# Performance work log

Measured on AMD Instinct MI355X. Metric: run time of the kernel, lower is better.

The kernel has to match this reference:

```python
import jax, jax.numpy as jnp
import numpy as np

N = 50000   # nodes
E = 800000  # edges (avg degree 16)
D = 128     # in = hidden = out channels (residual path active)
EPS = 1e-5  # BatchNorm eps


def setup_inputs() -> dict:
    key = jax.random.key(0)
    ks = jax.random.split(key, 24)
    sc = 1.0 / np.sqrt(D)
    inp = {
        "x": jax.random.normal(ks[0], (N, D), jnp.float32),
        "W1": jax.random.normal(ks[1], (D, D), jnp.float32) * sc,
        "b1": jnp.zeros((D,), jnp.float32),
        "g1": 1.0 + 0.1 * jax.random.normal(ks[2], (D,), jnp.float32),
        "be1": 0.1 * jax.random.normal(ks[3], (D,), jnp.float32),
        "m1": 0.1 * jax.random.normal(ks[4], (D,), jnp.float32),
        "v1": 0.5 + jax.random.uniform(ks[5], (D,), jnp.float32),
        "W2": jax.random.normal(ks[6], (D, D), jnp.float32) * sc,
        "b2": jnp.zeros((D,), jnp.float32),
        "g2": 1.0 + 0.1 * jax.random.normal(ks[7], (D,), jnp.float32),
        "be2": 0.1 * jax.random.normal(ks[8], (D,), jnp.float32),
        "m2": 0.1 * jax.random.normal(ks[9], (D,), jnp.float32),
        "v2": 0.5 + jax.random.uniform(ks[10], (D,), jnp.float32),
        "W3": jax.random.normal(ks[11], (D, D), jnp.float32) * sc,
        "b3": jnp.zeros((D,), jnp.float32),
        "src": jax.random.randint(ks[12], (E,), 0, N, jnp.int32),
        "dst": jax.random.randint(ks[13], (E,), 0, N, jnp.int32),
    }
    return inp


def _gcn_conv(x, W, b, src, dst):
    # PyG GCNConv: add self-loops, symmetric D^{-1/2}(A+I)D^{-1/2} normalization.
    h = x @ W                                              # [N, C]
    deg = jax.ops.segment_sum(jnp.ones((E,), x.dtype), dst, num_segments=N) + 1.0
    dinv = jax.lax.rsqrt(deg)                              # [N]
    coef = dinv[src] * dinv[dst]                           # [E]
    agg = jax.ops.segment_sum(h[src] * coef[:, None], dst, num_segments=N)
    agg = agg + h * (dinv * dinv)[:, None]                 # self-loop term
    return agg + b


def _bn(x, g, be, m, v):
    # eval-mode BatchNorm1d with running stats
    return (x - m) * jax.lax.rsqrt(v + EPS) * g + be


def reference(x, W1, b1, g1, be1, m1, v1, W2, b2, g2, be2, m2, v2, W3, b3, src, dst):
    x_res = x
    h = jax.nn.relu(_bn(_gcn_conv(x, W1, b1, src, dst), g1, be1, m1, v1))
    h = jax.nn.relu(_bn(_gcn_conv(h, W2, b2, src, dst), g2, be2, m2, v2))
    h = _gcn_conv(h, W3, b3, src, dst)
    return h + x_res  # in_channels == out_channels -> residual active
```

## Files before the change

### kernel.cpp

```cpp
#include <hip/hip_runtime.h>
#include <hip/hip_bf16.h>


#define GCN_N 50000
#define GCN_E 800000
#define GCN_D 128

__device__ __forceinline__ float bflo(unsigned u) { return __uint_as_float(u << 16); }
__device__ __forceinline__ float bfhi(unsigned u) { return __uint_as_float(u & 0xffff0000u); }
__device__ __forceinline__ unsigned f2bf(float f) {
    unsigned u = __float_as_uint(f);
    return (u + 0x7fffu + ((u >> 16) & 1u)) >> 16;
}

__global__ __launch_bounds__(256) void zero_kernel(int* __restrict__ p, int n) {
    int i = blockIdx.x * blockDim.x + threadIdx.x;
    if (i < n) p[i] = 0;
}

__global__ __launch_bounds__(256) void hist_kernel(const int* __restrict__ dst,
                                                   int* __restrict__ cnt, int nE) {
    int e = blockIdx.x * blockDim.x + threadIdx.x;
    if (e < nE) atomicAdd(&cnt[dst[e]], 1);
}

__global__ __launch_bounds__(256) void block_reduce(const int* __restrict__ cnt,
                                                    int* __restrict__ bsum, int n) {
    int tid = threadIdx.x, lane = tid & 63, wid = tid >> 6;
    int i0 = blockIdx.x * 1024 + tid * 4;
    int s = 0;
    #pragma unroll
    for (int q = 0; q < 4; ++q)
        if (i0 + q < n) s += cnt[i0 + q];
    #pragma unroll
    for (int off = 32; off >= 1; off >>= 1) s += __shfl_xor(s, off);
    __shared__ int ws[4];
    if (lane == 0) ws[wid] = s;
    __syncthreads();
    if (tid == 0) bsum[blockIdx.x] = ws[0] + ws[1] + ws[2] + ws[3];
}

__global__ void scan_bsums(const int* __restrict__ bsum, int* __restrict__ boff,
                           int nb, int* __restrict__ row_last) {
    int lane = threadIdx.x;
    int v = (lane < nb) ? bsum[lane] : 0;
    int sc = v;
    #pragma unroll
    for (int off = 1; off < 64; off <<= 1) {
        int t = __shfl_up(sc, off);
        if (lane >= off) sc += t;
    }
    if (lane < nb) boff[lane] = sc - v;
    if (lane == 63) *row_last = sc;
}

__global__ __launch_bounds__(256) void scan_apply(const int* __restrict__ cnt_in,
                                                  const int* __restrict__ boff,
                                                  int* __restrict__ row_ptr,
                                                  float* __restrict__ dinv,
                                                  int* __restrict__ cnt_zero, int n) {
    __shared__ int wsum[4];
    int tid = threadIdx.x, lane = tid & 63, wid = tid >> 6;
    int i0 = blockIdx.x * 1024 + tid * 4;
    int a0 = 0, a1 = 0, a2 = 0, a3 = 0;
    if (i0 + 0 < n) a0 = cnt_in[i0 + 0];
    if (i0 + 1 < n) a1 = cnt_in[i0 + 1];
    if (i0 + 2 < n) a2 = cnt_in[i0 + 2];
    if (i0 + 3 < n) a3 = cnt_in[i0 + 3];
    int tsum = a0 + a1 + a2 + a3;
    int sc = tsum;
    #pragma unroll
    for (int off = 1; off < 64; off <<= 1) {
        int t = __shfl_up(sc, off);
        if (lane >= off) sc += t;
    }
    if (lane == 63) wsum[wid] = sc;
    __syncthreads();
    int woff = 0;
    #pragma unroll
    for (int w = 0; w < 4; ++w)
        if (w < wid) woff += wsum[w];
    int excl = boff[blockIdx.x] + woff + (sc - tsum);
    if (i0 + 0 < n) { row_ptr[i0 + 0] = excl;                dinv[i0 + 0] = rsqrtf((float)a0 + 1.f); cnt_zero[i0 + 0] = 0; }
    if (i0 + 1 < n) { row_ptr[i0 + 1] = excl + a0;           dinv[i0 + 1] = rsqrtf((float)a1 + 1.f); cnt_zero[i0 + 1] = 0; }
    if (i0 + 2 < n) { row_ptr[i0 + 2] = excl + a0 + a1;      dinv[i0 + 2] = rsqrtf((float)a2 + 1.f); cnt_zero[i0 + 2] = 0; }
    if (i0 + 3 < n) { row_ptr[i0 + 3] = excl + a0 + a1 + a2; dinv[i0 + 3] = rsqrtf((float)a3 + 1.f); cnt_zero[i0 + 3] = 0; }
}

__global__ __launch_bounds__(256) void fill_kernel(const int* __restrict__ src,
                                                   const int* __restrict__ dst,
                                                   const int* __restrict__ row_ptr,
                                                   int* __restrict__ cur,
                                                   int* __restrict__ esrc, int nE) {
    int e = blockIdx.x * blockDim.x + threadIdx.x;
    if (e >= nE) return;
    int d = dst[e];
    int pos = row_ptr[d] + atomicAdd(&cur[d], 1);
    esrc[pos] = src[e];
}

__global__ void prep_kernel(const float* __restrict__ b, const float* __restrict__ g,
                            const float* __restrict__ be, const float* __restrict__ m,
                            const float* __restrict__ v, float* __restrict__ scale,
                            float* __restrict__ shift) {
    int c = threadIdx.x;
    float s = g[c] * rsqrtf(v[c] + 1e-5f);
    scale[c] = s;
    shift[c] = (b[c] - m[c]) * s + be[c];
}

__global__ __launch_bounds__(256) void mm_kernel(const float* __restrict__ A,
                                                 const float* __restrict__ W,
                                                 const float* __restrict__ dinv,
                                                 unsigned short* __restrict__ hb, int n) {
    __shared__ float As[64][68];
    __shared__ float Bs[64][132];
    int tid = threadIdx.x;
    int tx = tid & 15;
    int ty = tid >> 4;
    int row0 = blockIdx.x * 64;
    float acc[4][8] = {};

    for (int k0 = 0; k0 < 128; k0 += 64) {
        int ac = (tid & 15) * 4;
        int ar = tid >> 4;
        #pragma unroll
        for (int rr = 0; rr < 4; ++rr) {
            int r = ar + rr * 16;
            int gr = row0 + r;
            float4 v = make_float4(0.f, 0.f, 0.f, 0.f);
            if (gr < n) v = *(const float4*)&A[(size_t)gr * GCN_D + k0 + ac];
            *(float4*)&As[r][ac] = v;
        }
        int bc = (tid & 31) * 4;
        int br = tid >> 5;
        #pragma unroll
        for (int rr = 0; rr < 8; ++rr) {
            int r = br + rr * 8;
            float4 v = *(const float4*)&W[(size_t)(k0 + r) * GCN_D + bc];
            *(float4*)&Bs[r][bc] = v;
        }
        __syncthreads();
        #pragma unroll
        for (int kk = 0; kk < 64; ++kk) {
            float a[4];
            #pragma unroll
            for (int m = 0; m < 4; ++m) a[m] = As[ty * 4 + m][kk];
            float4 b0 = *(const float4*)&Bs[kk][tx * 8];
            float4 b1 = *(const float4*)&Bs[kk][tx * 8 + 4];
            float b[8] = {b0.x, b0.y, b0.z, b0.w, b1.x, b1.y, b1.z, b1.w};
            #pragma unroll
            for (int m = 0; m < 4; ++m)
                #pragma unroll
                for (int q = 0; q < 8; ++q) acc[m][q] += a[m] * b[q];
        }
        __syncthreads();
    }
    #pragma unroll
    for (int m = 0; m < 4; ++m) {
        int gr = row0 + ty * 4 + m;
        if (gr < n) {
            float dv = dinv[gr];
            unsigned w0 = f2bf(acc[m][0] * dv) | (f2bf(acc[m][1] * dv) << 16);
            unsigned w1 = f2bf(acc[m][2] * dv) | (f2bf(acc[m][3] * dv) << 16);
            unsigned w2 = f2bf(acc[m][4] * dv) | (f2bf(acc[m][5] * dv) << 16);
            unsigned w3 = f2bf(acc[m][6] * dv) | (f2bf(acc[m][7] * dv) << 16);
            *(uint4*)&hb[(size_t)gr * GCN_D + tx * 8] = make_uint4(w0, w1, w2, w3);
        }
    }
}

template <int FINAL>
__global__ __launch_bounds__(256) void agg_kernel(const unsigned short* __restrict__ hb,
                                                  const int* __restrict__ row_ptr,
                                                  const int* __restrict__ esrc,
                                                  const float* __restrict__ dinv,
                                                  const float* __restrict__ scale,
                                                  const float* __restrict__ shift,
                                                  const float* __restrict__ xres,
                                                  float* __restrict__ out, int n) {
    int wid = threadIdx.x >> 6, lane = threadIdx.x & 63;
    int node = blockIdx.x * 4 + wid;
    if (node >= n) return;
    int cc = lane * 2;
    unsigned us = *(const unsigned*)&hb[(size_t)node * GCN_D + cc];
    float aLo = bflo(us), aHi = bfhi(us);
    float bLo = 0.f, bHi = 0.f;
    int j = row_ptr[node], end = row_ptr[node + 1];
    for (; j + 8 <= end; j += 8) {
        int s0 = esrc[j + 0], s1 = esrc[j + 1], s2 = esrc[j + 2], s3 = esrc[j + 3];
        int s4 = esrc[j + 4], s5 = esrc[j + 5], s6 = esrc[j + 6], s7 = esrc[j + 7];
        unsigned u0 = *(const unsigned*)&hb[(size_t)s0 * GCN_D + cc];
        unsigned u1 = *(const unsigned*)&hb[(size_t)s1 * GCN_D + cc];
        unsigned u2 = *(const unsigned*)&hb[(size_t)s2 * GCN_D + cc];
        unsigned u3 = *(const unsigned*)&hb[(size_t)s3 * GCN_D + cc];
        unsigned u4 = *(const unsigned*)&hb[(size_t)s4 * GCN_D + cc];
        unsigned u5 = *(const unsigned*)&hb[(size_t)s5 * GCN_D + cc];
        unsigned u6 = *(const unsigned*)&hb[(size_t)s6 * GCN_D + cc];
        unsigned u7 = *(const unsigned*)&hb[(size_t)s7 * GCN_D + cc];
        aLo += bflo(u0) + bflo(u1);  aHi += bfhi(u0) + bfhi(u1);
        bLo += bflo(u2) + bflo(u3);  bHi += bfhi(u2) + bfhi(u3);
        aLo += bflo(u4) + bflo(u5);  aHi += bfhi(u4) + bfhi(u5);
        bLo += bflo(u6) + bflo(u7);  bHi += bfhi(u6) + bfhi(u7);
    }
    for (; j < end; ++j) {
        int s = esrc[j];
        unsigned u = *(const unsigned*)&hb[(size_t)s * GCN_D + cc];
        aLo += bflo(u);  aHi += bfhi(u);
    }
    float dvn = dinv[node];
    float vx = (aLo + bLo) * dvn;
    float vy = (aHi + bHi) * dvn;
    float2 o;
    if (FINAL) {
        float2 b = *(const float2*)&scale[cc];
        float2 xr = *(const float2*)&xres[(size_t)node * GCN_D + cc];
        o.x = vx + b.x + xr.x;
        o.y = vy + b.y + xr.y;
    } else {
        float2 sc = *(const float2*)&scale[cc];
        float2 sh = *(const float2*)&shift[cc];
        o.x = fmaxf(vx * sc.x + sh.x, 0.f);
        o.y = fmaxf(vy * sc.y + sh.y, 0.f);
    }
    *(float2*)&out[(size_t)node * GCN_D + cc] = o;
}

extern "C" void kernel_launch(void* const* d_in, const int* in_sizes, int n_in,
                              void* d_out, int out_size, void* d_ws, size_t ws_size,
                              hipStream_t stream) {
    (void)in_sizes; (void)n_in; (void)out_size; (void)ws_size;
    const int N = GCN_N, E = GCN_E, D = GCN_D;

    const float* x   = (const float*)d_in[0];
    const float* W1  = (const float*)d_in[1];
    const float* b1  = (const float*)d_in[2];
    const float* g1  = (const float*)d_in[3];
    const float* be1 = (const float*)d_in[4];
    const float* m1  = (const float*)d_in[5];
    const float* v1  = (const float*)d_in[6];
    const float* W2  = (const float*)d_in[7];
    const float* b2  = (const float*)d_in[8];
    const float* g2  = (const float*)d_in[9];
    const float* be2 = (const float*)d_in[10];
    const float* m2  = (const float*)d_in[11];
    const float* v2  = (const float*)d_in[12];
    const float* W3  = (const float*)d_in[13];
    const float* b3  = (const float*)d_in[14];
    const int* src   = (const int*)d_in[15];
    const int* dst   = (const int*)d_in[16];
    float* out = (float*)d_out;

    unsigned short* hb = (unsigned short*)d_ws;
    float* act    = (float*)(hb + (size_t)N * D);
    float* dinv   = act + (size_t)N * D;
    int* cnt      = (int*)(dinv + N);
    int* row_ptr  = cnt + N;
    int* esrc     = row_ptr + (N + 2);
    float* scale1 = (float*)(esrc + E);
    float* shift1 = scale1 + D;
    float* scale2 = shift1 + D;
    float* shift2 = scale2 + D;
    int* bsum     = (int*)(shift2 + D);
    int* boff     = bsum + 64;

    const int NB = (N + 1023) / 1024;

    zero_kernel<<<(N + 255) / 256, 256, 0, stream>>>(cnt, N);
    hist_kernel<<<(E + 255) / 256, 256, 0, stream>>>(dst, cnt, E);
    block_reduce<<<NB, 256, 0, stream>>>(cnt, bsum, N);
    scan_bsums<<<1, 64, 0, stream>>>(bsum, boff, NB, &row_ptr[N]);
    scan_apply<<<NB, 256, 0, stream>>>(cnt, boff, row_ptr, dinv, cnt, N);
    fill_kernel<<<(E + 255) / 256, 256, 0, stream>>>(src, dst, row_ptr, cnt, esrc, E);
    prep_kernel<<<1, D, 0, stream>>>(b1, g1, be1, m1, v1, scale1, shift1);
    prep_kernel<<<1, D, 0, stream>>>(b2, g2, be2, m2, v2, scale2, shift2);

    int mm_grid = (N + 63) / 64;
    int agg_grid = (N + 3) / 4;

    mm_kernel<<<mm_grid, 256, 0, stream>>>(x, W1, dinv, hb, N);
    agg_kernel<0><<<agg_grid, 256, 0, stream>>>(hb, row_ptr, esrc, dinv,
                                                scale1, shift1, nullptr, act, N);
    mm_kernel<<<mm_grid, 256, 0, stream>>>(act, W2, dinv, hb, N);
    agg_kernel<0><<<agg_grid, 256, 0, stream>>>(hb, row_ptr, esrc, dinv,
                                                scale2, shift2, nullptr, act, N);
    mm_kernel<<<mm_grid, 256, 0, stream>>>(act, W3, dinv, hb, N);
    agg_kernel<1><<<agg_grid, 256, 0, stream>>>(hb, row_ptr, esrc, dinv,
                                                b3, nullptr, x, out, N);
}
```

Baseline: 418.7 us.

## Use bf16 MFMA for dense transforms and store intermediate activations in bf16

Replaces the fp32 shared-memory SIMT GEMM with a kernel built on 16x16x32 bf16 MFMA instructions. The input x and the weights are cast to bf16 up front, with the weights stored transposed. The aggregation kernel now writes the hidden activations as bf16, which halves their write and read traffic. Accuracy drops because the GEMM inputs and activations are bf16, and the change adds four small prep launches plus an extra pass over x.

```diff
diff --git a/kernel.cpp b/kernel.cpp
--- a/kernel.cpp
+++ b/kernel.cpp
@@ -5,6 +5,9 @@
 #define GCN_N 50000
 #define GCN_E 800000
 #define GCN_D 128
+
+using bf16x8 = __attribute__((ext_vector_type(8))) short;
+using f32x4  = __attribute__((ext_vector_type(4))) float;
 
 __device__ __forceinline__ float bflo(unsigned u) { return __uint_as_float(u << 16); }
 __device__ __forceinline__ float bfhi(unsigned u) { return __uint_as_float(u & 0xffff0000u); }
@@ -109,64 +112,80 @@
     shift[c] = (b[c] - m[c]) * s + be[c];
 }
 
-__global__ __launch_bounds__(256) void mm_kernel(const float* __restrict__ A,
-                                                 const float* __restrict__ W,
-                                                 const float* __restrict__ dinv,
-                                                 unsigned short* __restrict__ hb, int n) {
-    __shared__ float As[64][68];
-    __shared__ float Bs[64][132];
+__global__ __launch_bounds__(256) void castx_kernel(const float* __restrict__ x,
+                                                    unsigned short* __restrict__ xb,
+                                                    int nElem) {
+    int i = (blockIdx.x * 256 + threadIdx.x) * 8;
+    if (i + 7 < nElem) {
+        float4 f0 = *(const float4*)&x[i];
+        float4 f1 = *(const float4*)&x[i + 4];
+        uint4 o;
+        o.x = f2bf(f0.x) | (f2bf(f0.y) << 16);
+        o.y = f2bf(f0.z) | (f2bf(f0.w) << 16);
+        o.z = f2bf(f1.x) | (f2bf(f1.y) << 16);
+        o.w = f2bf(f1.z) | (f2bf(f1.w) << 16);
+        *(uint4*)&xb[i] = o;
+    }
+}
+
+__global__ __launch_bounds__(256) void wtrans_kernel(const float* __restrict__ W,
+                                                     unsigned short* __restrict__ Wt) {
+    int id = blockIdx.x * 256 + threadIdx.x;
+    int nn = id >> 7, k = id & 127;
+    Wt[id] = (unsigned short)f2bf(W[k * 128 + nn]);
+}
+
+__global__ __launch_bounds__(256) void mm_mfma(const unsigned short* __restrict__ A,
+                                               const unsigned short* __restrict__ Wt,
+                                               const float* __restrict__ dinv,
+                                               unsigned short* __restrict__ hb, int n) {
+    __shared__ unsigned short Cs[64][136];
     int tid = threadIdx.x;
-    int tx = tid & 15;
-    int ty = tid >> 4;
+    int w = tid >> 6, l = tid & 63;
+    int lg = l >> 4, li = l & 15;
     int row0 = blockIdx.x * 64;
-    float acc[4][8] = {};
-
-    for (int k0 = 0; k0 < 128; k0 += 64) {
-        int ac = (tid & 15) * 4;
-        int ar = tid >> 4;
+
+    int arow = row0 + w * 16 + li;
+    int arow_c = min(arow, n - 1);
+    const unsigned short* ap = A + (size_t)arow_c * GCN_D + lg * 8;
+    bf16x8 a[4];
+    #pragma unroll
+    for (int k0 = 0; k0 < 4; ++k0) a[k0] = *(const bf16x8*)(ap + k0 * 32);
+
+    f32x4 acc[8];
+    #pragma unroll
+    for (int t = 0; t < 8; ++t) acc[t] = (f32x4){0.f, 0.f, 0.f, 0.f};
+
+    #pragma unroll
+    for (int t = 0; t < 8; ++t) {
+        const unsigned short* bp = Wt + (size_t)(t * 16 + li) * GCN_D + lg * 8;
         #pragma unroll
-        for (int rr = 0; rr < 4; ++rr) {
-            int r = ar + rr * 16;
-            int gr = row0 + r;
-            float4 v = make_float4(0.f, 0.f, 0.f, 0.f);
-            if (gr < n) v = *(const float4*)&A[(size_t)gr * GCN_D + k0 + ac];
-            *(float4*)&As[r][ac] = v;
+        for (int k0 = 0; k0 < 4; ++k0) {
+            bf16x8 b = *(const bf16x8*)(bp + k0 * 32);
+            acc[t] = __builtin_amdgcn_mfma_f32_16x16x32_bf16(a[k0], b, acc[t], 0, 0, 0);
         }
-        int bc = (tid & 31) * 4;
-        int br = tid >> 5;
+    }
+
+    int crow = w * 16 + lg * 4;
+    float dv[4];
+    #pragma unroll
+    for (int r = 0; r < 4; ++r) dv[r] = dinv[min(row0 + crow + r, n - 1)];
+    #pragma unroll
+    for (int t = 0; t < 8; ++t)
         #pragma unroll
-        for (int rr = 0; rr < 8; ++rr) {
-            int r = br + rr * 8;
-            float4 v = *(const float4*)&W[(size_t)(k0 + r) * GCN_D + bc];
-            *(float4*)&Bs[r][bc] = v;
-        }
-        __syncthreads();
-        #pragma unroll
-        for (int kk = 0; kk < 64; ++kk) {
-            float a[4];
-            #pragma unroll
-            for (int m = 0; m < 4; ++m) a[m] = As[ty * 4 + m][kk];
-            float4 b0 = *(const float4*)&Bs[kk][tx * 8];
-            float4 b1 = *(const float4*)&Bs[kk][tx * 8 + 4];
-            float b[8] = {b0.x, b0.y, b0.z, b0.w, b1.x, b1.y, b1.z, b1.w};
-            #pragma unroll
-            for (int m = 0; m < 4; ++m)
-                #pragma unroll
-                for (int q = 0; q < 8; ++q) acc[m][q] += a[m] * b[q];
-        }
-        __syncthreads();
-    }
-    #pragma unroll
-    for (int m = 0; m < 4; ++m) {
-        int gr = row0 + ty * 4 + m;
-        if (gr < n) {
-            float dv = dinv[gr];
-            unsigned w0 = f2bf(acc[m][0] * dv) | (f2bf(acc[m][1] * dv) << 16);
-            unsigned w1 = f2bf(acc[m][2] * dv) | (f2bf(acc[m][3] * dv) << 16);
-            unsigned w2 = f2bf(acc[m][4] * dv) | (f2bf(acc[m][5] * dv) << 16);
-            unsigned w3 = f2bf(acc[m][6] * dv) | (f2bf(acc[m][7] * dv) << 16);
-            *(uint4*)&hb[(size_t)gr * GCN_D + tx * 8] = make_uint4(w0, w1, w2, w3);
-        }
+        for (int r = 0; r < 4; ++r)
+            Cs[crow + r][t * 16 + li] = (unsigned short)f2bf(acc[t][r] * dv[r]);
+    __syncthreads();
+
+    int orow = tid >> 2;
+    int gr = row0 + orow;
+    if (gr < n) {
+        const unsigned short* sp = &Cs[orow][(tid & 3) * 32];
+        uint4* dp = (uint4*)&hb[(size_t)gr * GCN_D + (tid & 3) * 32];
+        dp[0] = *(const uint4*)(sp + 0);
+        dp[1] = *(const uint4*)(sp + 8);
+        dp[2] = *(const uint4*)(sp + 16);
+        dp[3] = *(const uint4*)(sp + 24);
     }
 }
 
@@ -178,7 +197,8 @@
                                                   const float* __restrict__ scale,
                                                   const float* __restrict__ shift,
                                                   const float* __restrict__ xres,
-                                                  float* __restrict__ out, int n) {
+                                                  unsigned short* __restrict__ outb,
+                                                  float* __restrict__ outf, int n) {
     int wid = threadIdx.x >> 6, lane = threadIdx.x & 63;
     int node = blockIdx.x * 4 + wid;
     if (node >= n) return;
@@ -211,19 +231,20 @@
     float dvn = dinv[node];
     float vx = (aLo + bLo) * dvn;
     float vy = (aHi + bHi) * dvn;
-    float2 o;
     if (FINAL) {
         float2 b = *(const float2*)&scale[cc];
         float2 xr = *(const float2*)&xres[(size_t)node * GCN_D + cc];
+        float2 o;
         o.x = vx + b.x + xr.x;
         o.y = vy + b.y + xr.y;
+        *(float2*)&outf[(size_t)node * GCN_D + cc] = o;
     } else {
         float2 sc = *(const float2*)&scale[cc];
         float2 sh = *(const float2*)&shift[cc];
-        o.x = fmaxf(vx * sc.x + sh.x, 0.f);
-        o.y = fmaxf(vy * sc.y + sh.y, 0.f);
-    }
-    *(float2*)&out[(size_t)node * GCN_D + cc] = o;
+        float ox = fmaxf(vx * sc.x + sh.x, 0.f);
+        float oy = fmaxf(vy * sc.y + sh.y, 0.f);
+        *(unsigned*)&outb[(size_t)node * GCN_D + cc] = f2bf(ox) | (f2bf(oy) << 16);
+    }
 }
 
 extern "C" void kernel_launch(void* const* d_in, const int* in_sizes, int n_in,
@@ -251,9 +272,13 @@
     const int* dst   = (const int*)d_in[16];
     float* out = (float*)d_out;
 
-    unsigned short* hb = (unsigned short*)d_ws;
-    float* act    = (float*)(hb + (size_t)N * D);
-    float* dinv   = act + (size_t)N * D;
+    unsigned short* hb   = (unsigned short*)d_ws;
+    unsigned short* actb = hb + (size_t)N * D;
+    unsigned short* xb   = actb + (size_t)N * D;
+    unsigned short* wt1  = xb + (size_t)N * D;
+    unsigned short* wt2  = wt1 + D * D;
+    unsigned short* wt3  = wt2 + D * D;
+    float* dinv   = (float*)(wt3 + D * D);
     int* cnt      = (int*)(dinv + N);
     int* row_ptr  = cnt + N;
     int* esrc     = row_ptr + (N + 2);
@@ -266,6 +291,10 @@
 
     const int NB = (N + 1023) / 1024;
 
+    castx_kernel<<<(N * D) / (256 * 8), 256, 0, stream>>>(x, xb, N * D);
+    wtrans_kernel<<<(D * D) / 256, 256, 0, stream>>>(W1, wt1);
+    wtrans_kernel<<<(D * D) / 256, 256, 0, stream>>>(W2, wt2);
+    wtrans_kernel<<<(D * D) / 256, 256, 0, stream>>>(W3, wt3);
     zero_kernel<<<(N + 255) / 256, 256, 0, stream>>>(cnt, N);
     hist_kernel<<<(E + 255) / 256, 256, 0, stream>>>(dst, cnt, E);
     block_reduce<<<NB, 256, 0, stream>>>(cnt, bsum, N);
@@ -278,13 +307,13 @@
     int mm_grid = (N + 63) / 64;
     int agg_grid = (N + 3) / 4;
 
-    mm_kernel<<<mm_grid, 256, 0, stream>>>(x, W1, dinv, hb, N);
+    mm_mfma<<<mm_grid, 256, 0, stream>>>(xb, wt1, dinv, hb, N);
     agg_kernel<0><<<agg_grid, 256, 0, stream>>>(hb, row_ptr, esrc, dinv,
-                                                scale1, shift1, nullptr, act, N);
-    mm_kernel<<<mm_grid, 256, 0, stream>>>(act, W2, dinv, hb, N);
+                                                scale1, shift1, nullptr, actb, nullptr, N);
+    mm_mfma<<<mm_grid, 256, 0, stream>>>(actb, wt2, dinv, hb, N);
     agg_kernel<0><<<agg_grid, 256, 0, stream>>>(hb, row_ptr, esrc, dinv,
-                                                scale2, shift2, nullptr, act, N);
-    mm_kernel<<<mm_grid, 256, 0, stream>>>(act, W3, dinv, hb, N);
+                                                scale2, shift2, nullptr, actb, nullptr, N);
+    mm_mfma<<<mm_grid, 256, 0, stream>>>(actb, wt3, dinv, hb, N);
     agg_kernel<1><<<agg_grid, 256, 0, stream>>>(hb, row_ptr, esrc, dinv,
-                                                b3, nullptr, x, out, N);
-}
+                                                b3, nullptr, x, nullptr, out, N);
+}
```

Result: faster. 393.0 us (-6.1%).
